# Kernel tuning notes

Measured on AMD Instinct MI355X. Metric: run time of the kernel, lower is better.

## Reference

```python
import jax, jax.numpy as jnp
import numpy as np

NUM_CODES = 100000
NUM_EDGES = 20000
DIM = 128
DEG = 32  # nodes per hyperedge -> 640000 incidences


def setup_inputs() -> dict:
    key = jax.random.key(0)
    k1, k2, k3, k4, k5 = jax.random.split(key, 5)
    n_inc = NUM_EDGES * DEG
    # incidence list: edge_ids is sorted (CSR-style), node_ids are member nodes
    node_ids = jax.random.randint(k1, (n_inc,), 0, NUM_CODES, dtype=jnp.int32)
    edge_ids = jnp.repeat(jnp.arange(NUM_EDGES, dtype=jnp.int32), DEG)
    # learned parameters (xavier-ish scales)
    node_emb = jax.random.normal(k2, (NUM_CODES, DIM), jnp.float32) * (1.0 / np.sqrt(DIM))
    edge_emb = jax.random.normal(k3, (NUM_EDGES, DIM), jnp.float32) * (1.0 / np.sqrt(DIM))
    W_e = jax.random.normal(k4, (DIM, DIM), jnp.float32) * (1.0 / np.sqrt(DIM))
    b_e = jnp.zeros((DIM,), jnp.float32)
    W_v = jax.random.normal(k5, (DIM, DIM), jnp.float32) * (1.0 / np.sqrt(DIM))
    b_v = jnp.zeros((DIM,), jnp.float32)
    return {"node_emb": node_emb, "edge_emb": edge_emb, "W_e": W_e, "b_e": b_e,
            "W_v": W_v, "b_v": b_v, "node_ids": node_ids, "edge_ids": edge_ids}


def reference(node_emb, edge_emb, W_e, b_e, W_v, b_v, node_ids, edge_ids):
    N, D = node_emb.shape
    E = edge_emb.shape[0]
    # node -> edge: mean of member node embeddings per hyperedge (segment mean)
    gathered = node_emb[node_ids]                                    # [I, D]
    seg_sum = jax.ops.segment_sum(gathered, edge_ids, num_segments=E)  # [E, D]
    seg_cnt = jax.ops.segment_sum(jnp.ones_like(edge_ids, jnp.float32), edge_ids, num_segments=E)
    mean = seg_sum / jnp.maximum(seg_cnt, 1.0)[:, None]
    # empty edges fall back to their own edge embedding (as in the torch loop)
    edge_ctx = jnp.where(seg_cnt[:, None] > 0, mean, edge_emb)
    edge_ctx = edge_ctx @ W_e.T + b_e                                # lin_e
    # edge -> node: scatter-add edge_ctx back to member nodes
    node_sum = jnp.zeros_like(node_emb).at[node_ids].add(edge_ctx[edge_ids])
    deg = jnp.zeros((N,), jnp.float32).at[node_ids].add(1.0)
    node_cnt = 1.0 + deg  # torch code clamps zeros to 1 BEFORE adding counts
    node_ctx = (node_sum / node_cnt[:, None]) @ W_v.T + b_v          # lin_v
    node_out = node_emb + node_ctx
    edge_out = edge_emb + edge_ctx
    return (node_out, edge_out)
```

## Files before the change

kernel.cpp:

```cpp
#include <hip/hip_runtime.h>

#define DIMS 128
#define DEG 32
#define CAP 32

typedef __attribute__((ext_vector_type(8))) short short8;
typedef __attribute__((ext_vector_type(4))) float floatx4;

static __device__ __forceinline__ unsigned short f2bf(float f) {
  unsigned int u = __float_as_uint(f);
  unsigned int r = (u + 0x7FFFu + ((u >> 16) & 1u)) >> 16;
  return (unsigned short)r;
}
static __device__ __forceinline__ float bf2f(unsigned short v) {
  return __uint_as_float(((unsigned int)v) << 16);
}

__global__ __launch_bounds__(256) void k_cvt_all(
    const float* __restrict__ a0, unsigned short* __restrict__ d0, int n0,
    const float* __restrict__ a1, unsigned short* __restrict__ d1, int n1,
    int* __restrict__ cnt, int ncnt) {
  int t = blockIdx.x * 256 + threadIdx.x;
  if (t < ncnt) cnt[t] = 0;
  int i = t * 4;
  const float* s; unsigned short* d;
  if (i < n0) { s = a0 + i; d = d0 + i; }
  else if (i < n0 + n1) { s = a1 + (i - n0); d = d1 + (i - n0); }
  else return;
  float4 v = *(const float4*)s;
  ushort4 o;
  o.x = f2bf(v.x); o.y = f2bf(v.y); o.z = f2bf(v.z); o.w = f2bf(v.w);
  *(ushort4*)d = o;
}

__global__ __launch_bounds__(256) void k_prep_wc(
    const float* __restrict__ Wv, const float* __restrict__ We,
    const float* __restrict__ be,
    unsigned short* __restrict__ Wc, float* __restrict__ bc) {
  int tid = threadIdx.x;
  if (blockIdx.x == 16) {
    __shared__ float be_s[DIMS];
    if (tid < DIMS) be_s[tid] = be[tid];
    __syncthreads();
    if (tid < DIMS) {
      float s = 0.f;
      for (int c = 0; c < DIMS; ++c) s += Wv[(size_t)tid * DIMS + c] * be_s[c];
      bc[tid] = s;
    }
    return;
  }
  __shared__ __align__(16) float We_s[DIMS][DIMS];
  __shared__ __align__(16) float wv_s[8][DIMS];
  int d0 = blockIdx.x * 8;
#pragma unroll
  for (int u = 0; u < 16; ++u) {
    int idx = tid + u * 256;
    int row = idx >> 5, c4 = idx & 31;
    *(float4*)&We_s[row][c4 * 4] = ((const float4*)We)[idx];
  }
  {
    int row = tid >> 5, c4 = tid & 31;
    *(float4*)&wv_s[row][c4 * 4] = ((const float4*)(Wv + (size_t)d0 * DIMS))[tid];
  }
  __syncthreads();
  int dd = tid >> 5;
  int k4 = (tid & 31) * 4;
  float4 acc = {0.f, 0.f, 0.f, 0.f};
  for (int c = 0; c < DIMS; ++c) {
    float w = wv_s[dd][c];
    float4 we = *(const float4*)&We_s[c][k4];
    acc.x += w * we.x; acc.y += w * we.y; acc.z += w * we.z; acc.w += w * we.w;
  }
  ushort4 o;
  o.x = f2bf(acc.x); o.y = f2bf(acc.y); o.z = f2bf(acc.z); o.w = f2bf(acc.w);
  *(ushort4*)(Wc + (size_t)(d0 + dd) * DIMS + k4) = o;
}

__global__ __launch_bounds__(256) void k_edge_fused(
    const unsigned short* __restrict__ node_emb_bf,
    const int* __restrict__ node_ids,
    const unsigned short* __restrict__ We,
    const unsigned short* __restrict__ Wc,
    const float* __restrict__ be,
    const float* __restrict__ bc,
    const float* __restrict__ edge_emb,
    float* __restrict__ edge_out,
    unsigned short* __restrict__ ectx2,
    int* __restrict__ cnt,
    unsigned short* __restrict__ bucket,
    int E) {
  int e0 = blockIdx.x * 16;
  int tid = threadIdx.x;
  __shared__ int ids[16][DEG];
  __shared__ __align__(16) unsigned short xs[16 * DIMS];
#pragma unroll
  for (int u = 0; u < 2; ++u) {
    int idx = tid + u * 256;
    int ee = idx >> 5, j = idx & 31;
    int e = e0 + ee;
    ids[ee][j] = (e < E) ? node_ids[(size_t)e * DEG + j] : 0;
  }
  __syncthreads();

  {
    int ee = tid >> 4;
    int l8 = tid & 15;
    float acc[8] = {0.f, 0.f, 0.f, 0.f, 0.f, 0.f, 0.f, 0.f};
#pragma unroll
    for (int jb = 0; jb < DEG; jb += 8) {
      short8 v[8];
#pragma unroll
      for (int u = 0; u < 8; ++u) {
        int n = ids[ee][jb + u];
        v[u] = *(const short8*)(node_emb_bf + (size_t)n * DIMS + l8 * 8);
      }
#pragma unroll
      for (int u = 0; u < 8; ++u)
#pragma unroll
        for (int t = 0; t < 8; ++t) acc[t] += bf2f((unsigned short)v[u][t]);
    }
    const float s = 1.0f / (float)DEG;
    short8 o;
#pragma unroll
    for (int t = 0; t < 8; ++t) o[t] = (short)f2bf(acc[t] * s);
    int byt = ee * 256 + ((l8 * 16) ^ ((ee & 7) << 4));
    *(short8*)((char*)xs + byt) = o;
  }

  {
    int ia = tid, ib = tid + 256;
    int ea = e0 + (ia >> 5), eb = e0 + (ib >> 5);
    int na = ids[ia >> 5][ia & 31];
    int nb = ids[ib >> 5][ib & 31];
    int pa = CAP, pb = CAP;
    bool va = ea < E, vb = eb < E;
    if (va) pa = atomicAdd(&cnt[na], 1);
    if (vb) pb = atomicAdd(&cnt[nb], 1);
    if (va && pa < CAP) bucket[(size_t)na * CAP + pa] = (unsigned short)ea;
    if (vb && pb < CAP) bucket[(size_t)nb * CAP + pb] = (unsigned short)eb;
  }
  __syncthreads();

  int wave = tid >> 6;
  int lane = tid & 63;
  int ln = lane & 15;
  int quad = lane >> 4;

  floatx4 acc_e0 = {0.f,0.f,0.f,0.f}, acc_e1 = {0.f,0.f,0.f,0.f};
  floatx4 acc_c0 = {0.f,0.f,0.f,0.f}, acc_c1 = {0.f,0.f,0.f,0.f};

#pragma unroll
  for (int kc = 0; kc < 4; ++kc) {
    int bofs = ln * 256 + ((kc * 64 + quad * 16) ^ ((ln & 7) << 4));
    short8 a = *(const short8*)((const char*)xs + bofs);
    int kb = kc * 32 + quad * 8;
    int wr0 = wave * 32 + ln;
    int wr1 = wave * 32 + 16 + ln;
    short8 bwe0 = *(const short8*)(We + (size_t)wr0 * DIMS + kb);
    short8 bwc0 = *(const short8*)(Wc + (size_t)wr0 * DIMS + kb);
    short8 bwe1 = *(const short8*)(We + (size_t)wr1 * DIMS + kb);
    short8 bwc1 = *(const short8*)(Wc + (size_t)wr1 * DIMS + kb);
    acc_e0 = __builtin_amdgcn_mfma_f32_16x16x32_bf16(bwe0, a, acc_e0, 0, 0, 0);
    acc_c0 = __builtin_amdgcn_mfma_f32_16x16x32_bf16(bwc0, a, acc_c0, 0, 0, 0);
    acc_e1 = __builtin_amdgcn_mfma_f32_16x16x32_bf16(bwe1, a, acc_e1, 0, 0, 0);
    acc_c1 = __builtin_amdgcn_mfma_f32_16x16x32_bf16(bwc1, a, acc_c1, 0, 0, 0);
  }

  int rE = e0 + ln;
  if (rE >= E) return;
#pragma unroll
  for (int t = 0; t < 2; ++t) {
    floatx4 ae = t ? acc_e1 : acc_e0;
    floatx4 ac = t ? acc_c1 : acc_c0;
    int c0 = wave * 32 + t * 16 + quad * 4;
    size_t off = (size_t)rE * DIMS + c0;
    float4 bev = *(const float4*)(be + c0);
    float4 rv = *(const float4*)(edge_emb + off);
    float4 ve;
    ve.x = ae[0] + bev.x + rv.x;
    ve.y = ae[1] + bev.y + rv.y;
    ve.z = ae[2] + bev.z + rv.z;
    ve.w = ae[3] + bev.w + rv.w;
    *(float4*)(edge_out + off) = ve;

    float4 bcv = *(const float4*)(bc + c0);
    ushort4 oc;
    oc.x = f2bf(ac[0] + bcv.x);
    oc.y = f2bf(ac[1] + bcv.y);
    oc.z = f2bf(ac[2] + bcv.z);
    oc.w = f2bf(ac[3] + bcv.w);
    *(ushort4*)(ectx2 + off) = oc;
  }
}

__global__ __launch_bounds__(256) void k_node_out(
    const unsigned short* __restrict__ ectx2,
    const unsigned short* __restrict__ bucket,
    const int* __restrict__ cnt,
    const unsigned short* __restrict__ node_emb_bf,
    const float* __restrict__ bv,
    float* __restrict__ node_out,
    int N) {
  int n0 = blockIdx.x * 16;
  int tid = threadIdx.x;
  __shared__ unsigned short elist[16][CAP];
  __shared__ float scale_s[16];
  __shared__ int cnt_s[16];
  {
    int nn = tid >> 4, p = tid & 15;
    int n = n0 + nn;
    unsigned int v = (n < N)
        ? ((const unsigned int*)(bucket + (size_t)n * CAP))[p] : 0u;
    elist[nn][p * 2] = (unsigned short)(v & 0xFFFFu);
    elist[nn][p * 2 + 1] = (unsigned short)(v >> 16);
  }
  if (tid < 16) {
    int n = n0 + tid;
    int c = (n < N) ? cnt[n] : 0;
    scale_s[tid] = 1.0f / (1.0f + (float)c);
    cnt_s[tid] = c > CAP ? CAP : c;
  }
  __syncthreads();
  int nn = tid >> 4;
  int l8 = tid & 15;
  int n = n0 + nn;
  if (n >= N) return;
  int c = cnt_s[nn];
  float acc[8] = {0.f, 0.f, 0.f, 0.f, 0.f, 0.f, 0.f, 0.f};
  int j = 0;
  for (; j + 4 <= c; j += 4) {
    short8 v0 = *(const short8*)(ectx2 + (size_t)elist[nn][j + 0] * DIMS + l8 * 8);
    short8 v1 = *(const short8*)(ectx2 + (size_t)elist[nn][j + 1] * DIMS + l8 * 8);
    short8 v2 = *(const short8*)(ectx2 + (size_t)elist[nn][j + 2] * DIMS + l8 * 8);
    short8 v3 = *(const short8*)(ectx2 + (size_t)elist[nn][j + 3] * DIMS + l8 * 8);
#pragma unroll
    for (int t = 0; t < 8; ++t)
      acc[t] += bf2f((unsigned short)v0[t]) + bf2f((unsigned short)v1[t]) +
                bf2f((unsigned short)v2[t]) + bf2f((unsigned short)v3[t]);
  }
  for (; j < c; ++j) {
    short8 v = *(const short8*)(ectx2 + (size_t)elist[nn][j] * DIMS + l8 * 8);
#pragma unroll
    for (int t = 0; t < 8; ++t) acc[t] += bf2f((unsigned short)v[t]);
  }
  float sc = scale_s[nn];
  short8 rb = *(const short8*)(node_emb_bf + (size_t)n * DIMS + l8 * 8);
  float4 bv0 = *(const float4*)(bv + l8 * 8);
  float4 bv1 = *(const float4*)(bv + l8 * 8 + 4);
  float4 o0, o1;
  o0.x = acc[0] * sc + bf2f((unsigned short)rb[0]) + bv0.x;
  o0.y = acc[1] * sc + bf2f((unsigned short)rb[1]) + bv0.y;
  o0.z = acc[2] * sc + bf2f((unsigned short)rb[2]) + bv0.z;
  o0.w = acc[3] * sc + bf2f((unsigned short)rb[3]) + bv0.w;
  o1.x = acc[4] * sc + bf2f((unsigned short)rb[4]) + bv1.x;
  o1.y = acc[5] * sc + bf2f((unsigned short)rb[5]) + bv1.y;
  o1.z = acc[6] * sc + bf2f((unsigned short)rb[6]) + bv1.z;
  o1.w = acc[7] * sc + bf2f((unsigned short)rb[7]) + bv1.w;
  float* dst = node_out + (size_t)n * DIMS + l8 * 8;
  *(float4*)dst = o0;
  *(float4*)(dst + 4) = o1;
}

extern "C" void kernel_launch(void* const* d_in, const int* in_sizes, int n_in,
                              void* d_out, int out_size, void* d_ws, size_t ws_size,
                              hipStream_t stream) {
  const float* node_emb = (const float*)d_in[0];
  const float* edge_emb = (const float*)d_in[1];
  const float* W_e      = (const float*)d_in[2];
  const float* b_e      = (const float*)d_in[3];
  const float* W_v      = (const float*)d_in[4];
  const float* b_v      = (const float*)d_in[5];
  const int*   node_ids = (const int*)d_in[6];

  const int N = in_sizes[0] / DIMS;
  const int E = in_sizes[1] / DIMS;

  float* out      = (float*)d_out;
  float* node_out = out;
  float* edge_out = out + (size_t)N * DIMS;

  unsigned short* nb    = (unsigned short*)d_ws;
  unsigned short* ectx2 = nb + (size_t)N * DIMS;
  unsigned short* web   = ectx2 + (size_t)E * DIMS;
  unsigned short* wcb   = web + DIMS * DIMS;
  float* bc  = (float*)(wcb + DIMS * DIMS);
  int* cntb   = (int*)(bc + DIMS);
  unsigned short* bucket = (unsigned short*)(cntb + N);

  int ntot = N * DIMS + DIMS * DIMS;
  k_cvt_all<<<(ntot / 4 + 255) / 256, 256, 0, stream>>>(
      node_emb, nb, N * DIMS, W_e, web, DIMS * DIMS, cntb, N);

  k_prep_wc<<<17, 256, 0, stream>>>(W_v, W_e, b_e, wcb, bc);

  k_edge_fused<<<(E + 15) / 16, 256, 0, stream>>>(
      nb, node_ids, web, wcb, b_e, bc, edge_emb, edge_out, ectx2,
      cntb, bucket, E);

  k_node_out<<<(N + 15) / 16, 256, 0, stream>>>(
      ectx2, bucket, cntb, nb, b_v, node_out, N);
}
```

Measured before the change: 200.1 us.

## Merge prep kernels, prefetch weights early, and batch first eight gathers in node kernel

Combines the bf16 conversion and Wc precompute into one launch, with the Wc blocks now reading W_e from global memory instead of staging a 64KB shared tile. In the edge kernel, weight fragments and the edge_emb residual are loaded before the gather phase, weights for the next k-step are double-buffered during the MFMA loop, and occupancy is hinted to 5 blocks per SM. The node kernel issues its residual loads early and always fetches the first eight edge rows at once, padding missing ones with a zero row appended to ectx2. These changes aim to cut one launch and hide memory latency, at the cost of extra register pressure and some wasted loads for low-degree nodes.

```diff
diff --git a/kernel.cpp b/kernel.cpp
--- a/kernel.cpp
+++ b/kernel.cpp
@@ -16,16 +16,57 @@
   return __uint_as_float(((unsigned int)v) << 16);
 }
 
-__global__ __launch_bounds__(256) void k_cvt_all(
-    const float* __restrict__ a0, unsigned short* __restrict__ d0, int n0,
-    const float* __restrict__ a1, unsigned short* __restrict__ d1, int n1,
-    int* __restrict__ cnt, int ncnt) {
-  int t = blockIdx.x * 256 + threadIdx.x;
+__global__ __launch_bounds__(256) void k_prep(
+    const float* __restrict__ node_emb, unsigned short* __restrict__ nb, int n0,
+    const float* __restrict__ We_f, unsigned short* __restrict__ web, int n1,
+    const float* __restrict__ Wv, const float* __restrict__ be,
+    unsigned short* __restrict__ Wc, float* __restrict__ bc,
+    int* __restrict__ cnt, int ncnt,
+    unsigned short* __restrict__ zrow) {
+  int b = blockIdx.x;
+  int tid = threadIdx.x;
+  if (b < 16) {
+    __shared__ __align__(16) float wv_s[8][DIMS];
+    int d0 = b * 8;
+    {
+      int row = tid >> 5, c4 = tid & 31;
+      *(float4*)&wv_s[row][c4 * 4] = ((const float4*)(Wv + (size_t)d0 * DIMS))[tid];
+    }
+    __syncthreads();
+    int dd = tid >> 5;
+    int k4 = (tid & 31) * 4;
+    float4 acc = {0.f, 0.f, 0.f, 0.f};
+    for (int c = 0; c < DIMS; ++c) {
+      float w = wv_s[dd][c];
+      float4 we = *(const float4*)(We_f + (size_t)c * DIMS + k4);
+      acc.x += w * we.x; acc.y += w * we.y; acc.z += w * we.z; acc.w += w * we.w;
+    }
+    ushort4 o;
+    o.x = f2bf(acc.x); o.y = f2bf(acc.y); o.z = f2bf(acc.z); o.w = f2bf(acc.w);
+    *(ushort4*)(Wc + (size_t)(d0 + dd) * DIMS + k4) = o;
+    return;
+  }
+  if (b == 16) {
+    __shared__ float be_s[DIMS];
+    if (tid < DIMS) be_s[tid] = be[tid];
+    if (tid >= 128 && tid < 144) {
+      short8 z = {0, 0, 0, 0, 0, 0, 0, 0};
+      *(short8*)(zrow + (size_t)(tid - 128) * 8) = z;
+    }
+    __syncthreads();
+    if (tid < DIMS) {
+      float s = 0.f;
+      for (int c = 0; c < DIMS; ++c) s += Wv[(size_t)tid * DIMS + c] * be_s[c];
+      bc[tid] = s;
+    }
+    return;
+  }
+  int t = (b - 17) * 256 + tid;
   if (t < ncnt) cnt[t] = 0;
   int i = t * 4;
   const float* s; unsigned short* d;
-  if (i < n0) { s = a0 + i; d = d0 + i; }
-  else if (i < n0 + n1) { s = a1 + (i - n0); d = d1 + (i - n0); }
+  if (i < n0) { s = node_emb + i; d = nb + i; }
+  else if (i < n0 + n1) { s = We_f + (i - n0); d = web + (i - n0); }
   else return;
   float4 v = *(const float4*)s;
   ushort4 o;
@@ -33,50 +74,7 @@
   *(ushort4*)d = o;
 }
 
-__global__ __launch_bounds__(256) void k_prep_wc(
-    const float* __restrict__ Wv, const float* __restrict__ We,
-    const float* __restrict__ be,
-    unsigned short* __restrict__ Wc, float* __restrict__ bc) {
-  int tid = threadIdx.x;
-  if (blockIdx.x == 16) {
-    __shared__ float be_s[DIMS];
-    if (tid < DIMS) be_s[tid] = be[tid];
-    __syncthreads();
-    if (tid < DIMS) {
-      float s = 0.f;
-      for (int c = 0; c < DIMS; ++c) s += Wv[(size_t)tid * DIMS + c] * be_s[c];
-      bc[tid] = s;
-    }
-    return;
-  }
-  __shared__ __align__(16) float We_s[DIMS][DIMS];
-  __shared__ __align__(16) float wv_s[8][DIMS];
-  int d0 = blockIdx.x * 8;
-#pragma unroll
-  for (int u = 0; u < 16; ++u) {
-    int idx = tid + u * 256;
-    int row = idx >> 5, c4 = idx & 31;
-    *(float4*)&We_s[row][c4 * 4] = ((const float4*)We)[idx];
-  }
-  {
-    int row = tid >> 5, c4 = tid & 31;
-    *(float4*)&wv_s[row][c4 * 4] = ((const float4*)(Wv + (size_t)d0 * DIMS))[tid];
-  }
-  __syncthreads();
-  int dd = tid >> 5;
-  int k4 = (tid & 31) * 4;
-  float4 acc = {0.f, 0.f, 0.f, 0.f};
-  for (int c = 0; c < DIMS; ++c) {
-    float w = wv_s[dd][c];
-    float4 we = *(const float4*)&We_s[c][k4];
-    acc.x += w * we.x; acc.y += w * we.y; acc.z += w * we.z; acc.w += w * we.w;
-  }
-  ushort4 o;
-  o.x = f2bf(acc.x); o.y = f2bf(acc.y); o.z = f2bf(acc.z); o.w = f2bf(acc.w);
-  *(ushort4*)(Wc + (size_t)(d0 + dd) * DIMS + k4) = o;
-}
-
-__global__ __launch_bounds__(256) void k_edge_fused(
+__global__ __launch_bounds__(256, 5) void k_edge_fused(
     const unsigned short* __restrict__ node_emb_bf,
     const int* __restrict__ node_ids,
     const unsigned short* __restrict__ We,
@@ -91,6 +89,24 @@
     int E) {
   int e0 = blockIdx.x * 16;
   int tid = threadIdx.x;
+  int wave = tid >> 6;
+  int lane = tid & 63;
+  int ln = lane & 15;
+  int quad = lane >> 4;
+  int wr0 = wave * 32 + ln;
+  int wr1 = wr0 + 16;
+
+  int kb0 = quad * 8;
+  short8 w_e0 = *(const short8*)(We + (size_t)wr0 * DIMS + kb0);
+  short8 w_c0 = *(const short8*)(Wc + (size_t)wr0 * DIMS + kb0);
+  short8 w_e1 = *(const short8*)(We + (size_t)wr1 * DIMS + kb0);
+  short8 w_c1 = *(const short8*)(Wc + (size_t)wr1 * DIMS + kb0);
+  int rE = e0 + ln;
+  int rEc = (rE < E) ? rE : (E - 1);
+  int cA = wave * 32 + quad * 4;
+  float4 emA = *(const float4*)(edge_emb + (size_t)rEc * DIMS + cA);
+  float4 emB = *(const float4*)(edge_emb + (size_t)rEc * DIMS + cA + 16);
+
   __shared__ int ids[16][DEG];
   __shared__ __align__(16) unsigned short xs[16 * DIMS];
 #pragma unroll
@@ -131,20 +147,15 @@
     int ia = tid, ib = tid + 256;
     int ea = e0 + (ia >> 5), eb = e0 + (ib >> 5);
     int na = ids[ia >> 5][ia & 31];
-    int nb = ids[ib >> 5][ib & 31];
+    int nb_ = ids[ib >> 5][ib & 31];
     int pa = CAP, pb = CAP;
     bool va = ea < E, vb = eb < E;
     if (va) pa = atomicAdd(&cnt[na], 1);
-    if (vb) pb = atomicAdd(&cnt[nb], 1);
+    if (vb) pb = atomicAdd(&cnt[nb_], 1);
     if (va && pa < CAP) bucket[(size_t)na * CAP + pa] = (unsigned short)ea;
-    if (vb && pb < CAP) bucket[(size_t)nb * CAP + pb] = (unsigned short)eb;
+    if (vb && pb < CAP) bucket[(size_t)nb_ * CAP + pb] = (unsigned short)eb;
   }
   __syncthreads();
-
-  int wave = tid >> 6;
-  int lane = tid & 63;
-  int ln = lane & 15;
-  int quad = lane >> 4;
 
   floatx4 acc_e0 = {0.f,0.f,0.f,0.f}, acc_e1 = {0.f,0.f,0.f,0.f};
   floatx4 acc_c0 = {0.f,0.f,0.f,0.f}, acc_c1 = {0.f,0.f,0.f,0.f};
@@ -153,42 +164,55 @@
   for (int kc = 0; kc < 4; ++kc) {
     int bofs = ln * 256 + ((kc * 64 + quad * 16) ^ ((ln & 7) << 4));
     short8 a = *(const short8*)((const char*)xs + bofs);
-    int kb = kc * 32 + quad * 8;
-    int wr0 = wave * 32 + ln;
-    int wr1 = wave * 32 + 16 + ln;
-    short8 bwe0 = *(const short8*)(We + (size_t)wr0 * DIMS + kb);
-    short8 bwc0 = *(const short8*)(Wc + (size_t)wr0 * DIMS + kb);
-    short8 bwe1 = *(const short8*)(We + (size_t)wr1 * DIMS + kb);
-    short8 bwc1 = *(const short8*)(Wc + (size_t)wr1 * DIMS + kb);
-    acc_e0 = __builtin_amdgcn_mfma_f32_16x16x32_bf16(bwe0, a, acc_e0, 0, 0, 0);
-    acc_c0 = __builtin_amdgcn_mfma_f32_16x16x32_bf16(bwc0, a, acc_c0, 0, 0, 0);
-    acc_e1 = __builtin_amdgcn_mfma_f32_16x16x32_bf16(bwe1, a, acc_e1, 0, 0, 0);
-    acc_c1 = __builtin_amdgcn_mfma_f32_16x16x32_bf16(bwc1, a, acc_c1, 0, 0, 0);
-  }
-
-  int rE = e0 + ln;
+    short8 n_e0, n_c0, n_e1, n_c1;
+    if (kc < 3) {
+      int kb = (kc + 1) * 32 + quad * 8;
+      n_e0 = *(const short8*)(We + (size_t)wr0 * DIMS + kb);
+      n_c0 = *(const short8*)(Wc + (size_t)wr0 * DIMS + kb);
+      n_e1 = *(const short8*)(We + (size_t)wr1 * DIMS + kb);
+      n_c1 = *(const short8*)(Wc + (size_t)wr1 * DIMS + kb);
+    }
+    acc_e0 = __builtin_amdgcn_mfma_f32_16x16x32_bf16(w_e0, a, acc_e0, 0, 0, 0);
+    acc_c0 = __builtin_amdgcn_mfma_f32_16x16x32_bf16(w_c0, a, acc_c0, 0, 0, 0);
+    acc_e1 = __builtin_amdgcn_mfma_f32_16x16x32_bf16(w_e1, a, acc_e1, 0, 0, 0);
+    acc_c1 = __builtin_amdgcn_mfma_f32_16x16x32_bf16(w_c1, a, acc_c1, 0, 0, 0);
+    if (kc < 3) { w_e0 = n_e0; w_c0 = n_c0; w_e1 = n_e1; w_c1 = n_c1; }
+  }
+
   if (rE >= E) return;
-#pragma unroll
-  for (int t = 0; t < 2; ++t) {
-    floatx4 ae = t ? acc_e1 : acc_e0;
-    floatx4 ac = t ? acc_c1 : acc_c0;
-    int c0 = wave * 32 + t * 16 + quad * 4;
-    size_t off = (size_t)rE * DIMS + c0;
-    float4 bev = *(const float4*)(be + c0);
-    float4 rv = *(const float4*)(edge_emb + off);
+  {
+    size_t off = (size_t)rE * DIMS + cA;
+    float4 bev = *(const float4*)(be + cA);
     float4 ve;
-    ve.x = ae[0] + bev.x + rv.x;
-    ve.y = ae[1] + bev.y + rv.y;
-    ve.z = ae[2] + bev.z + rv.z;
-    ve.w = ae[3] + bev.w + rv.w;
+    ve.x = acc_e0[0] + bev.x + emA.x;
+    ve.y = acc_e0[1] + bev.y + emA.y;
+    ve.z = acc_e0[2] + bev.z + emA.z;
+    ve.w = acc_e0[3] + bev.w + emA.w;
     *(float4*)(edge_out + off) = ve;
-
-    float4 bcv = *(const float4*)(bc + c0);
+    float4 bcv = *(const float4*)(bc + cA);
     ushort4 oc;
-    oc.x = f2bf(ac[0] + bcv.x);
-    oc.y = f2bf(ac[1] + bcv.y);
-    oc.z = f2bf(ac[2] + bcv.z);
-    oc.w = f2bf(ac[3] + bcv.w);
+    oc.x = f2bf(acc_c0[0] + bcv.x);
+    oc.y = f2bf(acc_c0[1] + bcv.y);
+    oc.z = f2bf(acc_c0[2] + bcv.z);
+    oc.w = f2bf(acc_c0[3] + bcv.w);
+    *(ushort4*)(ectx2 + off) = oc;
+  }
+  {
+    int c1 = cA + 16;
+    size_t off = (size_t)rE * DIMS + c1;
+    float4 bev = *(const float4*)(be + c1);
+    float4 ve;
+    ve.x = acc_e1[0] + bev.x + emB.x;
+    ve.y = acc_e1[1] + bev.y + emB.y;
+    ve.z = acc_e1[2] + bev.z + emB.z;
+    ve.w = acc_e1[3] + bev.w + emB.w;
+    *(float4*)(edge_out + off) = ve;
+    float4 bcv = *(const float4*)(bc + c1);
+    ushort4 oc;
+    oc.x = f2bf(acc_c1[0] + bcv.x);
+    oc.y = f2bf(acc_c1[1] + bcv.y);
+    oc.z = f2bf(acc_c1[2] + bcv.z);
+    oc.w = f2bf(acc_c1[3] + bcv.w);
     *(ushort4*)(ectx2 + off) = oc;
   }
 }
@@ -200,34 +224,50 @@
     const unsigned short* __restrict__ node_emb_bf,
     const float* __restrict__ bv,
     float* __restrict__ node_out,
-    int N) {
+    int N, int E) {
   int n0 = blockIdx.x * 16;
   int tid = threadIdx.x;
+  int nn = tid >> 4;
+  int l8 = tid & 15;
+  int n = n0 + nn;
+  int nc = (n < N) ? n : (N - 1);
+  short8 rb = *(const short8*)(node_emb_bf + (size_t)nc * DIMS + l8 * 8);
+  float4 bv0 = *(const float4*)(bv + l8 * 8);
+  float4 bv1 = *(const float4*)(bv + l8 * 8 + 4);
+
   __shared__ unsigned short elist[16][CAP];
   __shared__ float scale_s[16];
   __shared__ int cnt_s[16];
   {
-    int nn = tid >> 4, p = tid & 15;
-    int n = n0 + nn;
+    int p = tid & 15;
     unsigned int v = (n < N)
         ? ((const unsigned int*)(bucket + (size_t)n * CAP))[p] : 0u;
     elist[nn][p * 2] = (unsigned short)(v & 0xFFFFu);
     elist[nn][p * 2 + 1] = (unsigned short)(v >> 16);
   }
   if (tid < 16) {
-    int n = n0 + tid;
-    int c = (n < N) ? cnt[n] : 0;
+    int nq = n0 + tid;
+    int c = (nq < N) ? cnt[nq] : 0;
     scale_s[tid] = 1.0f / (1.0f + (float)c);
     cnt_s[tid] = c > CAP ? CAP : c;
   }
   __syncthreads();
-  int nn = tid >> 4;
-  int l8 = tid & 15;
-  int n = n0 + nn;
   if (n >= N) return;
   int c = cnt_s[nn];
   float acc[8] = {0.f, 0.f, 0.f, 0.f, 0.f, 0.f, 0.f, 0.f};
-  int j = 0;
+  {
+    short8 v[8];
+#pragma unroll
+    for (int u = 0; u < 8; ++u) {
+      int idx = (u < c) ? (int)elist[nn][u] : E;
+      v[u] = *(const short8*)(ectx2 + (size_t)idx * DIMS + l8 * 8);
+    }
+#pragma unroll
+    for (int u = 0; u < 8; ++u)
+#pragma unroll
+      for (int t = 0; t < 8; ++t) acc[t] += bf2f((unsigned short)v[u][t]);
+  }
+  int j = 8;
   for (; j + 4 <= c; j += 4) {
     short8 v0 = *(const short8*)(ectx2 + (size_t)elist[nn][j + 0] * DIMS + l8 * 8);
     short8 v1 = *(const short8*)(ectx2 + (size_t)elist[nn][j + 1] * DIMS + l8 * 8);
@@ -244,9 +284,6 @@
     for (int t = 0; t < 8; ++t) acc[t] += bf2f((unsigned short)v[t]);
   }
   float sc = scale_s[nn];
-  short8 rb = *(const short8*)(node_emb_bf + (size_t)n * DIMS + l8 * 8);
-  float4 bv0 = *(const float4*)(bv + l8 * 8);
-  float4 bv1 = *(const float4*)(bv + l8 * 8 + 4);
   float4 o0, o1;
   o0.x = acc[0] * sc + bf2f((unsigned short)rb[0]) + bv0.x;
   o0.y = acc[1] * sc + bf2f((unsigned short)rb[1]) + bv0.y;
@@ -281,22 +318,22 @@
 
   unsigned short* nb    = (unsigned short*)d_ws;
   unsigned short* ectx2 = nb + (size_t)N * DIMS;
-  unsigned short* web   = ectx2 + (size_t)E * DIMS;
+  unsigned short* web   = ectx2 + (size_t)(E + 1) * DIMS;
   unsigned short* wcb   = web + DIMS * DIMS;
   float* bc  = (float*)(wcb + DIMS * DIMS);
   int* cntb   = (int*)(bc + DIMS);
   unsigned short* bucket = (unsigned short*)(cntb + N);
 
   int ntot = N * DIMS + DIMS * DIMS;
-  k_cvt_all<<<(ntot / 4 + 255) / 256, 256, 0, stream>>>(
-      node_emb, nb, N * DIMS, W_e, web, DIMS * DIMS, cntb, N);
-
-  k_prep_wc<<<17, 256, 0, stream>>>(W_v, W_e, b_e, wcb, bc);
+  int nblk = 17 + (ntot / 4 + 255) / 256;
+  k_prep<<<nblk, 256, 0, stream>>>(
+      node_emb, nb, N * DIMS, W_e, web, DIMS * DIMS,
+      W_v, b_e, wcb, bc, cntb, N, ectx2 + (size_t)E * DIMS);
 
   k_edge_fused<<<(E + 15) / 16, 256, 0, stream>>>(
       nb, node_ids, web, wcb, b_e, bc, edge_emb, edge_out, ectx2,
       cntb, bucket, E);
 
   k_node_out<<<(N + 15) / 16, 256, 0, stream>>>(
-      ectx2, bucket, cntb, nb, b_v, node_out, N);
-}
+      ectx2, bucket, cntb, nb, b_v, node_out, N, E);
+}
```

Result: slower. 212.4 us (+6.2%).
